# Optimization experiments

Hardware: AMD Instinct MI355X
Metric: run time of the kernel (lower is better)

The kernel has to match this reference:

```python
import jax, jax.numpy as jnp
import numpy as np

B, T, D, H = 4, 2048, 1024, 16
Dh = D // H          # 64 head dim
NF = Dh // 2         # 32 rotary frequencies


def setup_inputs() -> dict:
    key = jax.random.key(0)
    k0, k1, k2, k3 = jax.random.split(key, 4)
    x = jax.random.normal(k0, (B, T, D), dtype=jnp.float32)
    # 3D spatial coordinates per token, e.g. voxel positions
    coords = jax.random.uniform(k1, (B, T, 3), dtype=jnp.float32, minval=0.0, maxval=64.0)
    w_scale = 1.0 / np.sqrt(D)
    qkv_w = jax.random.normal(k2, (3 * D, D), dtype=jnp.float32) * w_scale
    qkv_b = jnp.zeros((3 * D,), dtype=jnp.float32)
    proj_w = jax.random.normal(k3, (D, D), dtype=jnp.float32) * w_scale
    proj_b = jnp.zeros((D,), dtype=jnp.float32)
    # mixed-axis rope: frequency f uses coordinate axis (f % 3), geometric period spacing within each axis group
    axes = (jnp.arange(NF) % 3).astype(jnp.int32)
    group = (jnp.arange(NF) // 3).astype(jnp.float32)
    n_per_axis = float(NF) / 3.0
    inv_freq = (10000.0 ** (-group / n_per_axis)).astype(jnp.float32)
    return {"x": x, "coords": coords, "qkv_w": qkv_w, "qkv_b": qkv_b,
            "proj_w": proj_w, "proj_b": proj_b, "inv_freq": inv_freq, "axes": axes}


def _apply_rope(t, sin, cos):
    # t: [B, H, T, Dh]; sin/cos: [B, 1, T, Dh//2]  (rotate-half convention)
    t1, t2 = jnp.split(t, 2, axis=-1)
    return jnp.concatenate([t1 * cos - t2 * sin, t1 * sin + t2 * cos], axis=-1)


def reference(x, coords, qkv_w, qkv_b, proj_w, proj_b, inv_freq, axes):
    b, t, d = x.shape
    # fused QKV projection
    qkv = (x @ qkv_w.T + qkv_b).reshape(b, t, 3, H, Dh)
    qkv = jnp.transpose(qkv, (2, 0, 3, 1, 4))     # [3, B, H, T, Dh]
    q, k, v = qkv[0], qkv[1], qkv[2]
    # vectorized per-sample rope from coords (replaces python loop over batch)
    ang = jnp.take(coords, axes, axis=-1) * inv_freq      # [B, T, NF]
    sin = jnp.sin(ang)[:, None]                            # [B, 1, T, NF]
    cos = jnp.cos(ang)[:, None]
    q = _apply_rope(q, sin, cos)
    k = _apply_rope(k, sin, cos)
    # standard scaling mode: single 1/sqrt(Dh) inside SDPA
    scale = 1.0 / np.sqrt(Dh)
    scores = jnp.einsum('bhqd,bhkd->bhqk', q, k) * scale
    attn = jax.nn.softmax(scores, axis=-1)
    out = jnp.einsum('bhqk,bhkd->bhqd', attn, v)           # [B, H, T, Dh]
    out = jnp.transpose(out, (0, 2, 1, 3)).reshape(b, t, d)
    return out @ proj_w.T + proj_b
```

## Files before the change

kernel.cpp:

```cpp
#include <hip/hip_runtime.h>
#include <hip/hip_bf16.h>

#define B_ 4
#define T_ 2048
#define D_ 1024
#define H_ 16
#define DH 64
#define NF 32
#define BH (B_*H_)
#define M_ROWS (B_*T_)

using u16 = unsigned short;
using u32 = unsigned int;

typedef __bf16 bf16x8 __attribute__((ext_vector_type(8)));
typedef float  f32x4  __attribute__((ext_vector_type(4)));

__device__ __forceinline__ u16 f2bf(float f) {
  u32 u = __float_as_uint(f);
  u32 r = u + 0x7fffu + ((u >> 16) & 1u);
  return (u16)(r >> 16);
}
__device__ __forceinline__ u16 f2bf_hw(float f) {
  __bf16 h = (__bf16)f;
  return *(u16*)&h;
}
__device__ __forceinline__ float bf2f(u16 h) {
  return __uint_as_float(((u32)h) << 16);
}

__device__ __forceinline__ void gload_lds16(const void* g, void* l) {
  __builtin_amdgcn_global_load_lds((__attribute__((address_space(1))) void*)(g),
                                   (__attribute__((address_space(3))) void*)(l),
                                   16, 0, 0);
}

__global__ __launch_bounds__(256)
void cvt_kernel(const float* __restrict__ in, u16* __restrict__ out, int n8) {
  int idx = blockIdx.x * 256 + threadIdx.x;
  if (idx >= n8) return;
  const float4* p = (const float4*)in + (long)idx * 2;
  float4 a = p[0], b = p[1];
  u32 o0 = (u32)f2bf(a.x) | ((u32)f2bf(a.y) << 16);
  u32 o1 = (u32)f2bf(a.z) | ((u32)f2bf(a.w) << 16);
  u32 o2 = (u32)f2bf(b.x) | ((u32)f2bf(b.y) << 16);
  u32 o3 = (u32)f2bf(b.z) | ((u32)f2bf(b.w) << 16);
  ((uint4*)out)[idx] = make_uint4(o0, o1, o2, o3);
}

__global__ __launch_bounds__(256)
void sincos_kernel(const float* __restrict__ coords, const float* __restrict__ inv_freq,
                   const int* __restrict__ axes, float* __restrict__ sc) {
  int idx = blockIdx.x * 256 + threadIdx.x;
  if (idx >= B_ * T_ * NF) return;
  int f = idx & 31;
  long bt = idx >> 5;
  float c = coords[bt * 3 + axes[f]];
  float ang = c * inv_freq[f];
  sc[bt * 64 + f]      = sinf(ang);
  sc[bt * 64 + 32 + f] = cosf(ang);
}

template<int OUT_F32>
__global__ __launch_bounds__(256, 2)
void gemm_bt(const u16* __restrict__ A, const u16* __restrict__ Bt,
             const float* __restrict__ bias, void* __restrict__ Cout,
             int M, int N, int K) {
  __shared__ u16 As[128 * 64];
  __shared__ u16 Bs[128 * 64];
  int nb = N >> 7;
  int bid = blockIdx.x;
  int nwg = gridDim.x;
  if ((nwg & 7) == 0) {
    int c = nwg >> 3;
    bid = (bid & 7) * c + (bid >> 3);
  }
  int bm = bid / nb, bn = bid % nb;
  long m0 = (long)bm << 7, n0 = (long)bn << 7;
  int tid = threadIdx.x;
  int lane = tid & 63, w = tid >> 6;
  int g = lane >> 4, lr = lane & 15;
  int wm = w >> 1, wn = w & 1;

  f32x4 acc[4][4] = {};

  for (int kt = 0; kt < K; kt += 64) {
    __syncthreads();
    #pragma unroll
    for (int j = 0; j < 4; ++j) {
      int ob = j * 4096 + tid * 16;
      int row = ob >> 7, col = (ob & 127) >> 1;
      u16* ldsA = As + j * 2048 + w * 512;
      u16* ldsB = Bs + j * 2048 + w * 512;
      gload_lds16(A + (m0 + row) * K + kt + col, ldsA);
      gload_lds16(Bt + (n0 + row) * K + kt + col, ldsB);
    }
    __syncthreads();
    #pragma unroll
    for (int kk = 0; kk < 2; ++kk) {
      bf16x8 af[4], bfr[4];
      #pragma unroll
      for (int i = 0; i < 4; ++i)
        af[i] = *(const bf16x8*)(As + (wm * 64 + i * 16 + lr) * 64 + kk * 32 + g * 8);
      #pragma unroll
      for (int i = 0; i < 4; ++i)
        bfr[i] = *(const bf16x8*)(Bs + (wn * 64 + i * 16 + lr) * 64 + kk * 32 + g * 8);
      #pragma unroll
      for (int mi = 0; mi < 4; ++mi)
        #pragma unroll
        for (int nj = 0; nj < 4; ++nj)
          acc[mi][nj] = __builtin_amdgcn_mfma_f32_16x16x32_bf16(af[mi], bfr[nj], acc[mi][nj], 0, 0, 0);
    }
  }
  #pragma unroll
  for (int mi = 0; mi < 4; ++mi) {
    #pragma unroll
    for (int nj = 0; nj < 4; ++nj) {
      long col = n0 + wn * 64 + nj * 16 + lr;
      float bv = bias[col];
      #pragma unroll
      for (int i = 0; i < 4; ++i) {
        long row = m0 + wm * 64 + mi * 16 + g * 4 + i;
        float v = acc[mi][nj][i] + bv;
        if (OUT_F32) ((float*)Cout)[row * (long)N + col] = v;
        else         ((u16*)Cout)[row * (long)N + col] = f2bf(v);
      }
    }
  }
}

__global__ __launch_bounds__(256)
void rope_kernel(const u16* __restrict__ qkv, const float* __restrict__ sc,
                 u16* __restrict__ qr, u16* __restrict__ kr, u16* __restrict__ vt) {
  __shared__ u16 Vsm[128 * 72];
  int bh = blockIdx.y;
  int b = bh >> 4, h = bh & 15;
  int t0 = blockIdx.x << 7;
  int tid = threadIdx.x;

  #pragma unroll
  for (int part = 0; part < 2; ++part) {
    u16* outp = part ? kr : qr;
    float qscale = part ? 1.0f : 0.125f;
    #pragma unroll
    for (int it = 0; it < 2; ++it) {
      int item = it * 256 + tid;
      int tl = item >> 2, fg = item & 3;
      long t = t0 + tl;
      long rbase = ((long)(b * T_) + t) * 3072 + part * 1024 + h * 64 + fg * 8;
      uint4 u1 = *(const uint4*)(qkv + rbase);
      uint4 u2 = *(const uint4*)(qkv + rbase + 32);
      const float* scp = sc + ((long)(b * T_) + t) * 64 + fg * 8;
      float4 sn0 = *(const float4*)(scp);
      float4 sn1 = *(const float4*)(scp + 4);
      float4 cs0 = *(const float4*)(scp + 32);
      float4 cs1 = *(const float4*)(scp + 36);
      float sn[8], cs[8], f1[8], f2[8];
      u32 w1[4] = {u1.x, u1.y, u1.z, u1.w};
      u32 w2[4] = {u2.x, u2.y, u2.z, u2.w};
      #pragma unroll
      for (int j = 0; j < 4; ++j) {
        f1[2*j]   = bf2f((u16)(w1[j] & 0xffff));
        f1[2*j+1] = bf2f((u16)(w1[j] >> 16));
        f2[2*j]   = bf2f((u16)(w2[j] & 0xffff));
        f2[2*j+1] = bf2f((u16)(w2[j] >> 16));
      }
      sn[0]=sn0.x; sn[1]=sn0.y; sn[2]=sn0.z; sn[3]=sn0.w;
      sn[4]=sn1.x; sn[5]=sn1.y; sn[6]=sn1.z; sn[7]=sn1.w;
      cs[0]=cs0.x; cs[1]=cs0.y; cs[2]=cs0.z; cs[3]=cs0.w;
      cs[4]=cs1.x; cs[5]=cs1.y; cs[6]=cs1.z; cs[7]=cs1.w;
      u32 o1[4], o2[4];
      #pragma unroll
      for (int j = 0; j < 4; ++j) {
        u16 a0 = f2bf((f1[2*j]   * cs[2*j]   - f2[2*j]   * sn[2*j])   * qscale);
        u16 a1 = f2bf((f1[2*j+1] * cs[2*j+1] - f2[2*j+1] * sn[2*j+1]) * qscale);
        u16 b0 = f2bf((f1[2*j]   * sn[2*j]   + f2[2*j]   * cs[2*j])   * qscale);
        u16 b1 = f2bf((f1[2*j+1] * sn[2*j+1] + f2[2*j+1] * cs[2*j+1]) * qscale);
        o1[j] = (u32)a0 | ((u32)a1 << 16);
        o2[j] = (u32)b0 | ((u32)b1 << 16);
      }
      long obase = ((long)bh * T_ + t) * DH + fg * 8;
      *(uint4*)(outp + obase)      = make_uint4(o1[0], o1[1], o1[2], o1[3]);
      *(uint4*)(outp + obase + 32) = make_uint4(o2[0], o2[1], o2[2], o2[3]);
    }
  }
  #pragma unroll
  for (int it = 0; it < 4; ++it) {
    int item = it * 256 + tid;
    int tl = item >> 3, dg = item & 7;
    long t = t0 + tl;
    uint4 u = *(const uint4*)(qkv + ((long)(b * T_) + t) * 3072 + 2048 + h * 64 + dg * 8);
    *(uint4*)(Vsm + tl * 72 + dg * 8) = u;
  }
  __syncthreads();
  int d = tid >> 2, tc = tid & 3;
  long obase = ((long)bh * DH + d) * T_ + t0 + tc * 32;
  #pragma unroll
  for (int c = 0; c < 4; ++c) {
    u32 o[4];
    #pragma unroll
    for (int j = 0; j < 4; ++j) {
      u16 lo = Vsm[(tc * 32 + c * 8 + 2 * j)     * 72 + d];
      u16 hi = Vsm[(tc * 32 + c * 8 + 2 * j + 1) * 72 + d];
      o[j] = (u32)lo | ((u32)hi << 16);
    }
    *(uint4*)(vt + obase + c * 8) = make_uint4(o[0], o[1], o[2], o[3]);
  }
}

__global__ __launch_bounds__(256, 2)
void attn_kernel(const u16* __restrict__ Qr, const u16* __restrict__ Kr,
                 const u16* __restrict__ Vt, u16* __restrict__ Aout) {
  __shared__ u16 Ks[2][64 * 64];
  __shared__ u16 Vs[2][64 * 64];
  __shared__ u16 Ps[4][32 * 72];
  int bh = blockIdx.y;
  int b = bh >> 4, h = bh & 15;
  int q0 = blockIdx.x << 7;
  int tid = threadIdx.x;
  int lane = tid & 63, w = tid >> 6;
  int g = lane >> 4, lr = lane & 15;

  const long tbase = (long)bh * T_;
  const long vbase = (long)bh * DH;

  bf16x8 aq[2][2];
  #pragma unroll
  for (int mi = 0; mi < 2; ++mi)
    #pragma unroll
    for (int kk = 0; kk < 2; ++kk)
      aq[mi][kk] = *(const bf16x8*)(Qr + (tbase + q0 + w * 32 + mi * 16 + lr) * DH + kk * 32 + g * 8);

  f32x4 oacc[2][4] = {};
  float lsum[2][4] = {};

  const int swz0 = ((0 + g) ^ (lr & 7)) << 3;
  const int swz1 = ((4 + g) ^ (lr & 7)) << 3;

  auto STAGE = [&](int buf, int kb) {
    #pragma unroll
    for (int j = 0; j < 2; ++j) {
      int ob = j * 4096 + tid * 16;
      int row = ob >> 7;
      int c = ((ob >> 4) & 7) ^ (row & 7);
      u16* ldsK = Ks[buf] + j * 2048 + w * 512;
      u16* ldsV = Vs[buf] + j * 2048 + w * 512;
      gload_lds16(Kr + (tbase + kb + row) * DH + c * 8, ldsK);
      gload_lds16(Vt + (vbase + row) * T_ + kb + c * 8, ldsV);
    }
  };

  STAGE(0, 0);
  asm volatile("s_waitcnt vmcnt(0)" ::: "memory");
  __builtin_amdgcn_s_barrier();
  __builtin_amdgcn_sched_barrier(0);

  int cur = 0;
  for (int kt = 0; kt < T_ / 64; ++kt) {
    if (kt + 1 < T_ / 64) STAGE(cur ^ 1, (kt + 1) * 64);

    const u16* kbuf = Ks[cur];
    const u16* vbuf = Vs[cur];

    f32x4 s[2][4] = {};
    #pragma unroll
    for (int kk = 0; kk < 2; ++kk) {
      int so = kk ? swz1 : swz0;
      bf16x8 bk[4];
      #pragma unroll
      for (int nj = 0; nj < 4; ++nj)
        bk[nj] = *(const bf16x8*)(kbuf + (nj * 16 + lr) * 64 + so);
      #pragma unroll
      for (int mi = 0; mi < 2; ++mi)
        #pragma unroll
        for (int nj = 0; nj < 4; ++nj)
          s[mi][nj] = __builtin_amdgcn_mfma_f32_16x16x32_bf16(aq[mi][kk], bk[nj], s[mi][nj], 0, 0, 0);
    }

    u16* pw = Ps[w];
    #pragma unroll
    for (int mi = 0; mi < 2; ++mi) {
      #pragma unroll
      for (int i = 0; i < 4; ++i) {
        float p0 = __expf(s[mi][0][i]);
        float p1 = __expf(s[mi][1][i]);
        float p2 = __expf(s[mi][2][i]);
        float p3 = __expf(s[mi][3][i]);
        lsum[mi][i] += (p0 + p1) + (p2 + p3);
        int rb = (mi * 16 + g * 4 + i) * 72 + lr;
        pw[rb]      = f2bf_hw(p0);
        pw[rb + 16] = f2bf_hw(p1);
        pw[rb + 32] = f2bf_hw(p2);
        pw[rb + 48] = f2bf_hw(p3);
      }
    }
    asm volatile("s_waitcnt lgkmcnt(0)" ::: "memory");
    __builtin_amdgcn_sched_barrier(0);

    #pragma unroll
    for (int kk = 0; kk < 2; ++kk) {
      int so = kk ? swz1 : swz0;
      bf16x8 ap[2], bv[4];
      #pragma unroll
      for (int mi = 0; mi < 2; ++mi)
        ap[mi] = *(const bf16x8*)(pw + (mi * 16 + lr) * 72 + kk * 32 + g * 8);
      #pragma unroll
      for (int nj = 0; nj < 4; ++nj)
        bv[nj] = *(const bf16x8*)(vbuf + (nj * 16 + lr) * 64 + so);
      #pragma unroll
      for (int mi = 0; mi < 2; ++mi)
        #pragma unroll
        for (int nj = 0; nj < 4; ++nj)
          oacc[mi][nj] = __builtin_amdgcn_mfma_f32_16x16x32_bf16(ap[mi], bv[nj], oacc[mi][nj], 0, 0, 0);
    }

    __builtin_amdgcn_sched_barrier(0);
    asm volatile("s_waitcnt vmcnt(0)" ::: "memory");
    __builtin_amdgcn_s_barrier();
    __builtin_amdgcn_sched_barrier(0);
    cur ^= 1;
  }

  #pragma unroll
  for (int mi = 0; mi < 2; ++mi) {
    #pragma unroll
    for (int i = 0; i < 4; ++i) {
      float l = lsum[mi][i];
      #pragma unroll
      for (int dd = 1; dd < 16; dd <<= 1) l += __shfl_xor(l, dd);
      float inv = 1.0f / l;
      long q = q0 + w * 32 + mi * 16 + g * 4 + i;
      long obase = ((long)b * T_ + q) * D_ + h * DH;
      #pragma unroll
      for (int nj = 0; nj < 4; ++nj)
        Aout[obase + nj * 16 + lr] = f2bf_hw(oacc[mi][nj][i] * inv);
    }
  }
}

extern "C" void kernel_launch(void* const* d_in, const int* in_sizes, int n_in,
                              void* d_out, int out_size, void* d_ws, size_t ws_size,
                              hipStream_t stream) {
  const float* x        = (const float*)d_in[0];
  const float* coords   = (const float*)d_in[1];
  const float* qkv_w    = (const float*)d_in[2];
  const float* qkv_b    = (const float*)d_in[3];
  const float* proj_w   = (const float*)d_in[4];
  const float* proj_b   = (const float*)d_in[5];
  const float* inv_freq = (const float*)d_in[6];
  const int*   axes     = (const int*)d_in[7];
  float* out = (float*)d_out;

  char* ws = (char*)d_ws;
  size_t off = 0;
  auto alloc = [&](size_t bytes) -> char* {
    char* p = ws + off;
    off += (bytes + 255) & ~(size_t)255;
    return p;
  };
  u16*   xb     = (u16*)  alloc((size_t)M_ROWS * D_ * 2);
  u16*   wqkv   = (u16*)  alloc((size_t)3 * D_ * D_ * 2);
  u16*   wproj  = (u16*)  alloc((size_t)D_ * D_ * 2);
  float* sc     = (float*)alloc((size_t)M_ROWS * 64 * 4);
  u16*   qkvraw = (u16*)  alloc((size_t)M_ROWS * 3 * D_ * 2);
  u16*   qr     = (u16*)  alloc((size_t)BH * T_ * DH * 2);
  u16*   kr     = (u16*)  alloc((size_t)BH * T_ * DH * 2);
  u16*   vt     = (u16*)  alloc((size_t)BH * T_ * DH * 2);
  u16*   aout   = qkvraw;

  cvt_kernel<<<(M_ROWS * D_ / 8 + 255) / 256, 256, 0, stream>>>(x, xb, M_ROWS * D_ / 8);
  cvt_kernel<<<(3 * D_ * D_ / 8 + 255) / 256, 256, 0, stream>>>(qkv_w, wqkv, 3 * D_ * D_ / 8);
  cvt_kernel<<<(D_ * D_ / 8 + 255) / 256, 256, 0, stream>>>(proj_w, wproj, D_ * D_ / 8);
  sincos_kernel<<<(B_ * T_ * NF + 255) / 256, 256, 0, stream>>>(coords, inv_freq, axes, sc);

  gemm_bt<0><<<(M_ROWS / 128) * (3 * D_ / 128), 256, 0, stream>>>(xb, wqkv, qkv_b, qkvraw,
                                                                  M_ROWS, 3 * D_, D_);
  rope_kernel<<<dim3(T_ / 128, BH), 256, 0, stream>>>(qkvraw, sc, qr, kr, vt);
  attn_kernel<<<dim3(T_ / 128, BH), 256, 0, stream>>>(qr, kr, vt, aout);
  gemm_bt<1><<<(M_ROWS / 128) * (D_ / 128), 256, 0, stream>>>(aout, wproj, proj_b, out,
                                                              M_ROWS, D_, D_);
}
```

Baseline: 234.8 us.

## Process two query blocks per attention workgroup, use exp2 with folded log2e

Each attention workgroup now handles 256 queries (two 128-query sub-blocks), so every staged K/V tile is reused for twice as many queries and global K/V traffic per query is halved. The grid becomes 512 one-dimensional blocks, remapped so that blocks placed on the same XCD handle related heads. log2(e) is folded into the Q scale in the rope kernel so the softmax can call exp2 instead of exp. The trade-offs are more registers for the doubled Q fragments and accumulators, and half as many workgroups, which lowers parallelism.

After: 256.4 us. +9.2%, slower.

```diff
diff --git a/kernel.cpp b/kernel.cpp
--- a/kernel.cpp
+++ b/kernel.cpp
@@ -141,7 +141,7 @@
   #pragma unroll
   for (int part = 0; part < 2; ++part) {
     u16* outp = part ? kr : qr;
-    float qscale = part ? 1.0f : 0.125f;
+    float qscale = part ? 1.0f : 0.125f * 1.44269504088896f;
     #pragma unroll
     for (int it = 0; it < 2; ++it) {
       int item = it * 256 + tid;
@@ -214,9 +214,10 @@
   __shared__ u16 Ks[2][64 * 64];
   __shared__ u16 Vs[2][64 * 64];
   __shared__ u16 Ps[4][32 * 72];
-  int bh = blockIdx.y;
+  int wg = (blockIdx.x & 7) * 64 + (blockIdx.x >> 3);
+  int bh = wg >> 3;
   int b = bh >> 4, h = bh & 15;
-  int q0 = blockIdx.x << 7;
+  int q0 = (wg & 7) << 8;
   int tid = threadIdx.x;
   int lane = tid & 63, w = tid >> 6;
   int g = lane >> 4, lr = lane & 15;
@@ -224,15 +225,18 @@
   const long tbase = (long)bh * T_;
   const long vbase = (long)bh * DH;
 
-  bf16x8 aq[2][2];
-  #pragma unroll
-  for (int mi = 0; mi < 2; ++mi)
-    #pragma unroll
-    for (int kk = 0; kk < 2; ++kk)
-      aq[mi][kk] = *(const bf16x8*)(Qr + (tbase + q0 + w * 32 + mi * 16 + lr) * DH + kk * 32 + g * 8);
-
-  f32x4 oacc[2][4] = {};
-  float lsum[2][4] = {};
+  bf16x8 aq[2][2][2];
+  #pragma unroll
+  for (int qb = 0; qb < 2; ++qb)
+    #pragma unroll
+    for (int mi = 0; mi < 2; ++mi)
+      #pragma unroll
+      for (int kk = 0; kk < 2; ++kk)
+        aq[qb][mi][kk] = *(const bf16x8*)(Qr + (tbase + q0 + qb * 128 + w * 32 + mi * 16 + lr) * DH
+                                          + kk * 32 + g * 8);
+
+  f32x4 oacc[2][2][4] = {};
+  float lsum[2][2][4] = {};
 
   const int swz0 = ((0 + g) ^ (lr & 7)) << 3;
   const int swz1 = ((4 + g) ^ (lr & 7)) << 3;
@@ -261,57 +265,60 @@
 
     const u16* kbuf = Ks[cur];
     const u16* vbuf = Vs[cur];
-
-    f32x4 s[2][4] = {};
-    #pragma unroll
-    for (int kk = 0; kk < 2; ++kk) {
-      int so = kk ? swz1 : swz0;
-      bf16x8 bk[4];
-      #pragma unroll
-      for (int nj = 0; nj < 4; ++nj)
-        bk[nj] = *(const bf16x8*)(kbuf + (nj * 16 + lr) * 64 + so);
-      #pragma unroll
-      for (int mi = 0; mi < 2; ++mi)
+    u16* pw = Ps[w];
+
+    #pragma unroll
+    for (int qb = 0; qb < 2; ++qb) {
+      f32x4 s[2][4] = {};
+      #pragma unroll
+      for (int kk = 0; kk < 2; ++kk) {
+        int so = kk ? swz1 : swz0;
+        bf16x8 bk[4];
         #pragma unroll
         for (int nj = 0; nj < 4; ++nj)
-          s[mi][nj] = __builtin_amdgcn_mfma_f32_16x16x32_bf16(aq[mi][kk], bk[nj], s[mi][nj], 0, 0, 0);
-    }
-
-    u16* pw = Ps[w];
-    #pragma unroll
-    for (int mi = 0; mi < 2; ++mi) {
-      #pragma unroll
-      for (int i = 0; i < 4; ++i) {
-        float p0 = __expf(s[mi][0][i]);
-        float p1 = __expf(s[mi][1][i]);
-        float p2 = __expf(s[mi][2][i]);
-        float p3 = __expf(s[mi][3][i]);
-        lsum[mi][i] += (p0 + p1) + (p2 + p3);
-        int rb = (mi * 16 + g * 4 + i) * 72 + lr;
-        pw[rb]      = f2bf_hw(p0);
-        pw[rb + 16] = f2bf_hw(p1);
-        pw[rb + 32] = f2bf_hw(p2);
-        pw[rb + 48] = f2bf_hw(p3);
-      }
-    }
-    asm volatile("s_waitcnt lgkmcnt(0)" ::: "memory");
-    __builtin_amdgcn_sched_barrier(0);
-
-    #pragma unroll
-    for (int kk = 0; kk < 2; ++kk) {
-      int so = kk ? swz1 : swz0;
-      bf16x8 ap[2], bv[4];
-      #pragma unroll
-      for (int mi = 0; mi < 2; ++mi)
-        ap[mi] = *(const bf16x8*)(pw + (mi * 16 + lr) * 72 + kk * 32 + g * 8);
-      #pragma unroll
-      for (int nj = 0; nj < 4; ++nj)
-        bv[nj] = *(const bf16x8*)(vbuf + (nj * 16 + lr) * 64 + so);
-      #pragma unroll
-      for (int mi = 0; mi < 2; ++mi)
+          bk[nj] = *(const bf16x8*)(kbuf + (nj * 16 + lr) * 64 + so);
+        #pragma unroll
+        for (int mi = 0; mi < 2; ++mi)
+          #pragma unroll
+          for (int nj = 0; nj < 4; ++nj)
+            s[mi][nj] = __builtin_amdgcn_mfma_f32_16x16x32_bf16(aq[qb][mi][kk], bk[nj], s[mi][nj], 0, 0, 0);
+      }
+
+      #pragma unroll
+      for (int mi = 0; mi < 2; ++mi) {
+        #pragma unroll
+        for (int i = 0; i < 4; ++i) {
+          float p0 = __builtin_exp2f(s[mi][0][i]);
+          float p1 = __builtin_exp2f(s[mi][1][i]);
+          float p2 = __builtin_exp2f(s[mi][2][i]);
+          float p3 = __builtin_exp2f(s[mi][3][i]);
+          lsum[qb][mi][i] += (p0 + p1) + (p2 + p3);
+          int rb = (mi * 16 + g * 4 + i) * 72 + lr;
+          pw[rb]      = f2bf_hw(p0);
+          pw[rb + 16] = f2bf_hw(p1);
+          pw[rb + 32] = f2bf_hw(p2);
+          pw[rb + 48] = f2bf_hw(p3);
+        }
+      }
+      asm volatile("s_waitcnt lgkmcnt(0)" ::: "memory");
+      __builtin_amdgcn_sched_barrier(0);
+
+      #pragma unroll
+      for (int kk = 0; kk < 2; ++kk) {
+        int so = kk ? swz1 : swz0;
+        bf16x8 ap[2], bv[4];
+        #pragma unroll
+        for (int mi = 0; mi < 2; ++mi)
+          ap[mi] = *(const bf16x8*)(pw + (mi * 16 + lr) * 72 + kk * 32 + g * 8);
         #pragma unroll
         for (int nj = 0; nj < 4; ++nj)
-          oacc[mi][nj] = __builtin_amdgcn_mfma_f32_16x16x32_bf16(ap[mi], bv[nj], oacc[mi][nj], 0, 0, 0);
+          bv[nj] = *(const bf16x8*)(vbuf + (nj * 16 + lr) * 64 + so);
+        #pragma unroll
+        for (int mi = 0; mi < 2; ++mi)
+          #pragma unroll
+          for (int nj = 0; nj < 4; ++nj)
+            oacc[qb][mi][nj] = __builtin_amdgcn_mfma_f32_16x16x32_bf16(ap[mi], bv[nj], oacc[qb][mi][nj], 0, 0, 0);
+      }
     }
 
     __builtin_amdgcn_sched_barrier(0);
@@ -322,18 +329,21 @@
   }
 
   #pragma unroll
-  for (int mi = 0; mi < 2; ++mi) {
-    #pragma unroll
-    for (int i = 0; i < 4; ++i) {
-      float l = lsum[mi][i];
-      #pragma unroll
-      for (int dd = 1; dd < 16; dd <<= 1) l += __shfl_xor(l, dd);
-      float inv = 1.0f / l;
-      long q = q0 + w * 32 + mi * 16 + g * 4 + i;
-      long obase = ((long)b * T_ + q) * D_ + h * DH;
-      #pragma unroll
-      for (int nj = 0; nj < 4; ++nj)
-        Aout[obase + nj * 16 + lr] = f2bf_hw(oacc[mi][nj][i] * inv);
+  for (int qb = 0; qb < 2; ++qb) {
+    #pragma unroll
+    for (int mi = 0; mi < 2; ++mi) {
+      #pragma unroll
+      for (int i = 0; i < 4; ++i) {
+        float l = lsum[qb][mi][i];
+        #pragma unroll
+        for (int dd = 1; dd < 16; dd <<= 1) l += __shfl_xor(l, dd);
+        float inv = 1.0f / l;
+        long q = q0 + qb * 128 + w * 32 + mi * 16 + g * 4 + i;
+        long obase = ((long)b * T_ + q) * D_ + h * DH;
+        #pragma unroll
+        for (int nj = 0; nj < 4; ++nj)
+          Aout[obase + nj * 16 + lr] = f2bf_hw(oacc[qb][mi][nj][i] * inv);
+      }
     }
   }
 }
@@ -376,7 +386,7 @@
   gemm_bt<0><<<(M_ROWS / 128) * (3 * D_ / 128), 256, 0, stream>>>(xb, wqkv, qkv_b, qkvraw,
                                                                   M_ROWS, 3 * D_, D_);
   rope_kernel<<<dim3(T_ / 128, BH), 256, 0, stream>>>(qkvraw, sc, qr, kr, vt);
-  attn_kernel<<<dim3(T_ / 128, BH), 256, 0, stream>>>(qr, kr, vt, aout);
+  attn_kernel<<<512, 256, 0, stream>>>(qr, kr, vt, aout);
   gemm_bt<1><<<(M_ROWS / 128) * (D_ / 128), 256, 0, stream>>>(aout, wproj, proj_b, out,
                                                               M_ROWS, D_, D_);
 }
```
